# Optimization experiments

Hardware: AMD Instinct MI355X
Metric: run time of the kernel (lower is better)

Reference implementation:

```python
import jax, jax.numpy as jnp
import numpy as np

VIOL_TOL = 12.0
CLASH_TOL = 1.5
C_N_LEN = (1.329, 1.341)        # (non-proline, proline)
C_N_STD = (0.014, 0.016)
CA_C_N = (-0.5203, 0.0353)      # (gt cos, stddev)
C_N_CA = (-0.4473, 0.0311)
EPS = 1e-6


def setup_inputs() -> dict:
    key = jax.random.key(0)
    k = jax.random.split(key, 6)
    B, N = 1, 512
    pos = jax.random.normal(k[0], (B, N, 14, 3), jnp.float32) * 5.0
    atom_mask = jnp.ones((B, N, 14), jnp.float32)
    residue_types = jax.random.randint(k[1], (B, N), 0, 21, dtype=jnp.int32)
    residue_index = jnp.broadcast_to(jnp.arange(N, dtype=jnp.int32)[None], (B, N))
    vdw_table = jax.random.uniform(k[2], (21, 14), jnp.float32, 1.0, 2.0)
    lower_bound_table = jax.random.uniform(k[3], (21, 14, 14), jnp.float32, 1.0, 2.0)
    upper_bound_table = lower_bound_table + jax.random.uniform(k[4], (21, 14, 14), jnp.float32, 0.5, 1.5)
    return {
        'predicted_positions': pos,
        'atom_mask': atom_mask,
        'residue_types': residue_types,
        'residue_index': residue_index,
        'vdw_table': vdw_table,
        'lower_bound_table': lower_bound_table,
        'upper_bound_table': upper_bound_table,
    }


def _bond_angle_losses(pos, atom_mask, residue_types, residue_index):
    f32 = pos.dtype
    this_ca, this_ca_m = pos[:, :-1, 1, :], atom_mask[:, :-1, 1]
    this_c, this_c_m = pos[:, :-1, 2, :], atom_mask[:, :-1, 2]
    next_n, next_n_m = pos[:, 1:, 0, :], atom_mask[:, 1:, 0]
    next_ca, next_ca_m = pos[:, 1:, 1, :], atom_mask[:, 1:, 1]
    no_gap = (residue_index[:, 1:] - residue_index[:, :-1] == 1).astype(f32)

    c_n_len = jnp.sqrt(jnp.sum((this_c - next_n) ** 2, -1) + EPS)
    pro = (residue_types[:, 1:] == 14).astype(f32)
    gt_len = (1.0 - pro) * C_N_LEN[0] + pro * C_N_LEN[1]
    gt_std = (1.0 - pro) * C_N_STD[0] + pro * C_N_STD[1]
    c_n_mask = this_c_m * next_n_m * no_gap
    c_n_err = jnp.sqrt((c_n_len - gt_len) ** 2 + EPS)
    c_n_loss = jnp.sum(c_n_mask * jax.nn.relu(c_n_err - VIOL_TOL * gt_std), -1) / (jnp.sum(c_n_mask, -1) + EPS)

    ca_c_len = jnp.sqrt(jnp.sum((this_ca - this_c) ** 2, -1) + EPS)
    n_ca_len = jnp.sqrt(jnp.sum((next_n - next_ca) ** 2, -1) + EPS)
    c_ca_u = (this_ca - this_c) / ca_c_len[..., None]
    c_n_u = (next_n - this_c) / c_n_len[..., None]
    n_ca_u = (next_ca - next_n) / n_ca_len[..., None]

    ca_c_n = jnp.sum(c_ca_u * c_n_u, -1)
    ca_c_n_mask = this_ca_m * this_c_m * next_n_m * no_gap
    ca_c_n_err = jnp.sqrt((ca_c_n - CA_C_N[0]) ** 2 + EPS)
    ca_c_n_loss = jnp.sum(ca_c_n_mask * jax.nn.relu(ca_c_n_err - VIOL_TOL * CA_C_N[1]), -1) / (jnp.sum(ca_c_n_mask, -1) + EPS)

    c_n_ca = jnp.sum(-c_n_u * n_ca_u, -1)
    c_n_ca_mask = this_c_m * next_n_m * next_ca_m * no_gap
    c_n_ca_err = jnp.sqrt((c_n_ca - C_N_CA[0]) ** 2 + EPS)
    c_n_ca_loss = jnp.sum(c_n_ca_mask * jax.nn.relu(c_n_ca_err - VIOL_TOL * C_N_CA[1]), -1) / (jnp.sum(c_n_ca_mask, -1) + EPS)

    return c_n_loss, ca_c_n_loss, c_n_ca_loss


def _clash_per_atom(pos, atom_mask, residue_types, residue_index, vdw_table):
    f32 = pos.dtype
    B, N = pos.shape[:2]
    A = N * 14
    pos_f = pos.reshape(B, A, 3)
    m_f = atom_mask.reshape(B, A)
    rt = jnp.minimum(residue_types, 20)
    vdw_f = vdw_table[rt].reshape(B, A)  # gather [B,N,14] -> flat

    diff = pos_f[:, :, None, :] - pos_f[:, None, :, :]
    dist = jnp.sqrt(jnp.sum(diff ** 2, -1) + 1e-8)  # [B,A,A]

    pair = m_f[:, :, None] * m_f[:, None, :]
    ari = jnp.repeat(residue_index, 14, axis=1)  # atom residue index [B,A]
    pair = pair * (ari[:, :, None] < ari[:, None, :]).astype(f32)

    slot = jnp.tile(jnp.arange(14), N)[None]  # [1,A]
    rtf = jnp.repeat(residue_types, 14, axis=1)
    c_n_bond = ((slot[:, :, None] == 2) & (slot[:, None, :] == 0) & (ari[:, None, :] - ari[:, :, None] == 1)) | \
               ((slot[:, :, None] == 0) & (slot[:, None, :] == 2) & (ari[:, :, None] - ari[:, None, :] == 1))
    disulfide = (rtf[:, :, None] == 4) & (rtf[:, None, :] == 4) & (slot[:, :, None] == 5) & (slot[:, None, :] == 5)
    pair = pair * (~c_n_bond).astype(f32) * (~disulfide).astype(f32)

    vdw_sum = vdw_f[:, :, None] + vdw_f[:, None, :]
    clash = jax.nn.relu(vdw_sum - CLASH_TOL - dist) * pair
    per_atom = (jnp.sum(clash, axis=1) + jnp.sum(clash, axis=2)).reshape(B, N, 14)
    return per_atom


def _within_per_atom(pos, atom_mask, residue_types, lower_bound_table, upper_bound_table):
    f32 = pos.dtype
    rt = jnp.minimum(residue_types, 20)
    lb = lower_bound_table[rt]  # [B,N,14,14]
    ub = upper_bound_table[rt]
    d = jnp.sqrt(jnp.sum((pos[:, :, :, None, :] - pos[:, :, None, :, :]) ** 2, -1) + 1e-8)
    pair = atom_mask[:, :, :, None] * atom_mask[:, :, None, :]
    pair = pair * (1.0 - jnp.eye(14, dtype=f32)[None, None])
    pair = pair * ((lb > 0.0) | (ub > 0.0)).astype(f32)
    loss = (jax.nn.relu(lb - d) + jax.nn.relu(d - ub)) * pair
    return jnp.sum(loss, axis=-2) + jnp.sum(loss, axis=-1)  # [B,N,14]


def reference(predicted_positions, atom_mask, residue_types, residue_index,
              vdw_table, lower_bound_table, upper_bound_table):
    c_n, ca_c_n, c_n_ca = _bond_angle_losses(predicted_positions, atom_mask, residue_types, residue_index)
    clash_pa = _clash_per_atom(predicted_positions, atom_mask, residue_types, residue_index, vdw_table)
    within_pa = _within_per_atom(predicted_positions, atom_mask, residue_types, lower_bound_table, upper_bound_table)
    num_atoms = jnp.clip(jnp.sum(atom_mask, axis=(1, 2)), 1e-6, None)
    clash_loss = jnp.sum(clash_pa + within_pa, axis=(1, 2)) / num_atoms
    return c_n + ca_c_n + c_n_ca + clash_loss
```

## Files before the change

kernel.cpp:

```cpp
#include <hip/hip_runtime.h>

#define EPS 1e-6f
#define IT 512
#define JTL 64
#define RATIO 8
#define WB 64

static __device__ __forceinline__ float wave_reduce_add(float v) {
#pragma unroll
    for (int o = 32; o > 0; o >>= 1) v += __shfl_down(v, o, 64);
    return v;
}


__device__ void do_bonds(const float* __restrict__ P, const float* __restrict__ M,
                         const int* __restrict__ RT, const int* __restrict__ RI,
                         float* __restrict__ Wtail, int N) {
    float n0 = 0.f, de0 = 0.f, n1 = 0.f, de1 = 0.f, n2 = 0.f, de2 = 0.f;
    for (int i = threadIdx.x; i < N - 1; i += blockDim.x) {
        float no_gap = (RI[i + 1] - RI[i] == 1) ? 1.f : 0.f;
        const float* ca0 = P + i * 42 + 3;
        const float* c0  = P + i * 42 + 6;
        const float* nn  = P + (i + 1) * 42 + 0;
        const float* ca1 = P + (i + 1) * 42 + 3;
        float m_ca0 = M[i * 14 + 1], m_c0 = M[i * 14 + 2];
        float m_nn = M[(i + 1) * 14 + 0], m_ca1 = M[(i + 1) * 14 + 1];

        float bx = nn[0] - c0[0], by = nn[1] - c0[1], bz = nn[2] - c0[2];
        float c_n_len = sqrtf(bx * bx + by * by + bz * bz + EPS);
        float pro = (RT[i + 1] == 14) ? 1.f : 0.f;
        float gt_len = (1.f - pro) * 1.329f + pro * 1.341f;
        float gt_std = (1.f - pro) * 0.014f + pro * 0.016f;
        float cnm = m_c0 * m_nn * no_gap;
        float dl = c_n_len - gt_len;
        float cne = sqrtf(dl * dl + EPS);
        n0 += cnm * fmaxf(cne - 12.f * gt_std, 0.f);
        de0 += cnm;

        float ax = ca0[0] - c0[0], ay = ca0[1] - c0[1], az = ca0[2] - c0[2];
        float ca_c_len = sqrtf(ax * ax + ay * ay + az * az + EPS);
        float ex = ca1[0] - nn[0], ey = ca1[1] - nn[1], ez = ca1[2] - nn[2];
        float n_ca_len = sqrtf(ex * ex + ey * ey + ez * ez + EPS);
        float inv_cn = 1.f / c_n_len, inv_ac = 1.f / ca_c_len, inv_nc = 1.f / n_ca_len;
        float ux = bx * inv_cn, uy = by * inv_cn, uz = bz * inv_cn;
        float cx = ax * inv_ac, cy = ay * inv_ac, cz = az * inv_ac;
        float wx = ex * inv_nc, wy = ey * inv_nc, wz = ez * inv_nc;

        float cacn = cx * ux + cy * uy + cz * uz;
        float m1 = m_ca0 * m_c0 * m_nn * no_gap;
        float t1 = cacn + 0.5203f;
        float e1 = sqrtf(t1 * t1 + EPS);
        n1 += m1 * fmaxf(e1 - 12.f * 0.0353f, 0.f);
        de1 += m1;

        float cnca = -(ux * wx + uy * wy + uz * wz);
        float m2 = m_c0 * m_nn * m_ca1 * no_gap;
        float t2 = cnca + 0.4473f;
        float e2 = sqrtf(t2 * t2 + EPS);
        n2 += m2 * fmaxf(e2 - 12.f * 0.0311f, 0.f);
        de2 += m2;
    }
    n0 = wave_reduce_add(n0); de0 = wave_reduce_add(de0);
    n1 = wave_reduce_add(n1); de1 = wave_reduce_add(de1);
    n2 = wave_reduce_add(n2); de2 = wave_reduce_add(de2);
    __shared__ float red[24];
    int lane = threadIdx.x & 63, wid = threadIdx.x >> 6;
    if (lane == 0) {
        red[wid * 6 + 0] = n0; red[wid * 6 + 1] = de0; red[wid * 6 + 2] = n1;
        red[wid * 6 + 3] = de1; red[wid * 6 + 4] = n2; red[wid * 6 + 5] = de2;
    }
    __syncthreads();
    if (threadIdx.x < 6) {
        Wtail[threadIdx.x] = red[threadIdx.x] + red[6 + threadIdx.x]
                           + red[12 + threadIdx.x] + red[18 + threadIdx.x];
    }
}

__device__ void do_within(const float* __restrict__ pos, const float* __restrict__ am,
                          const int* __restrict__ rtypes,
                          const float* __restrict__ lbt, const float* __restrict__ ubt,
                          float* __restrict__ slot, int N, int b, int wblk) {
    int total = N * 196;
    float sum = 0.f;
    for (int idx = wblk * blockDim.x + threadIdx.x; idx < total; idx += WB * blockDim.x) {
        int n = idx / 196;
        int p = idx - n * 196;
        int i = p / 14;
        int j = p - i * 14;
        if (i == j) continue;
        size_t bn = (size_t)b * N + n;
        int rt = rtypes[bn]; rt = rt < 20 ? rt : 20;
        const float* pi = pos + bn * 42 + i * 3;
        const float* pj = pos + bn * 42 + j * 3;
        float dx = pi[0] - pj[0], dy = pi[1] - pj[1], dz = pi[2] - pj[2];
        float d = sqrtf(dx * dx + dy * dy + dz * dz + 1e-8f);
        float lb = lbt[rt * 196 + p], ub = ubt[rt * 196 + p];
        float gate = (lb > 0.f || ub > 0.f) ? 1.f : 0.f;
        float m = am[bn * 14 + i] * am[bn * 14 + j] * gate;
        sum += (fmaxf(lb - d, 0.f) + fmaxf(d - ub, 0.f)) * m;
    }
    sum = wave_reduce_add(sum);
    __shared__ float red2[4];
    int lane = threadIdx.x & 63, wid = threadIdx.x >> 6;
    if (lane == 0) red2[wid] = sum;
    __syncthreads();
    if (threadIdx.x == 0) *slot = red2[0] + red2[1] + red2[2] + red2[3];
}

__device__ void do_clash(const float* __restrict__ P, const float* __restrict__ M,
                         const int* __restrict__ RT, const int* __restrict__ RI,
                         const float* __restrict__ vdw, float* __restrict__ slot,
                         int N, int A, int TJ, int p) {
    int bi = 0, rem = p;
    while (true) {
        int cnt = TJ - RATIO * bi;
        cnt = cnt > 0 ? cnt : 0;
        if (rem < cnt) break;
        rem -= cnt; ++bi;
    }
    int bj = RATIO * bi + rem;

    __shared__ float4 sPos[JTL];
    __shared__ float sMask[JTL];
    __shared__ int sRI[JTL];
    __shared__ int sMeta[JTL];

    int t = threadIdx.x;
    if (t < JTL) {
        int j = bj * JTL + t;
        if (j < A) {
            int res = j / 14;
            int sl = j - res * 14;
            int rt = RT[res];
            int rtc = rt < 20 ? rt : 20;
            sPos[t] = make_float4(P[j * 3], P[j * 3 + 1], P[j * 3 + 2],
                                  vdw[rtc * 14 + sl] - 1.5f);
            sMask[t] = M[j];
            sRI[t] = RI[res];
            sMeta[t] = sl | (((rt == 4) && (sl == 5)) ? 16 : 0);
        } else {
            sPos[t] = make_float4(1e30f, 1e30f, 1e30f, -1e30f);
            sMask[t] = 0.f; sRI[t] = 0x7fffffff; sMeta[t] = 0;
        }
    }
    __syncthreads();

    int i0 = bi * IT + t;
    int i1 = i0 + 256;
    float xi0 = 0.f, yi0 = 0.f, zi0 = 0.f, vi0 = -1e30f, mi0 = 0.f;
    float xi1 = 0.f, yi1 = 0.f, zi1 = 0.f, vi1 = -1e30f, mi1 = 0.f;
    int iri0 = 0, iri1 = 0;
    bool icys0 = false, icys1 = false;
    int isl0 = -1, isl1 = -1;
    if (i0 < A) {
        int res = i0 / 14; isl0 = i0 - res * 14;
        int rt = RT[res]; int rtc = rt < 20 ? rt : 20;
        vi0 = vdw[rtc * 14 + isl0];
        xi0 = P[i0 * 3]; yi0 = P[i0 * 3 + 1]; zi0 = P[i0 * 3 + 2];
        mi0 = M[i0]; iri0 = RI[res]; icys0 = (rt == 4) && (isl0 == 5);
        if (mi0 == 0.f) vi0 = -1e30f;
    }
    if (i1 < A) {
        int res = i1 / 14; isl1 = i1 - res * 14;
        int rt = RT[res]; int rtc = rt < 20 ? rt : 20;
        vi1 = vdw[rtc * 14 + isl1];
        xi1 = P[i1 * 3]; yi1 = P[i1 * 3 + 1]; zi1 = P[i1 * 3 + 2];
        mi1 = M[i1]; iri1 = RI[res]; icys1 = (rt == 4) && (isl1 == 5);
        if (mi1 == 0.f) vi1 = -1e30f;
    }

    float sum = 0.f;
    int jbase_g = bj * JTL;
    for (int base = 0; base < JTL; base += 8) {
        float4 r[8];
#pragma unroll
        for (int k = 0; k < 8; ++k) r[k] = sPos[base + k];
#pragma unroll
        for (int k = 0; k < 8; ++k) {
            float w = r[k].w;
            {
                float dx = xi0 - r[k].x, dy = yi0 - r[k].y, dz = zi0 - r[k].z;
                float d2 = dx * dx + dy * dy + dz * dz;
                float s = vi0 + w;
                if (s > 0.f && d2 < s * s) {
                    int jj = base + k, jg = jbase_g + jj;
                    if (i0 < jg) {
                        int jri = sRI[jj];
                        if (iri0 != jri) {
                            int dj = jri - iri0;
                            int jm = sMeta[jj], jsl = jm & 15;
                            bool cn = (isl0 == 2 && jsl == 0 && dj == 1) ||
                                      (isl0 == 0 && jsl == 2 && dj == -1);
                            bool ssb = icys0 && (jm & 16);
                            if (!cn && !ssb)
                                sum += (s - sqrtf(d2 + 1e-8f)) * mi0 * sMask[jj];
                        }
                    }
                }
            }
            {
                float dx = xi1 - r[k].x, dy = yi1 - r[k].y, dz = zi1 - r[k].z;
                float d2 = dx * dx + dy * dy + dz * dz;
                float s = vi1 + w;
                if (s > 0.f && d2 < s * s) {
                    int jj = base + k, jg = jbase_g + jj;
                    if (i1 < jg) {
                        int jri = sRI[jj];
                        if (iri1 != jri) {
                            int dj = jri - iri1;
                            int jm = sMeta[jj], jsl = jm & 15;
                            bool cn = (isl1 == 2 && jsl == 0 && dj == 1) ||
                                      (isl1 == 0 && jsl == 2 && dj == -1);
                            bool ssb = icys1 && (jm & 16);
                            if (!cn && !ssb)
                                sum += (s - sqrtf(d2 + 1e-8f)) * mi1 * sMask[jj];
                        }
                    }
                }
            }
        }
    }
    sum = wave_reduce_add(sum);
    __shared__ float red3[4];
    int lane = t & 63, wid = t >> 6;
    if (lane == 0) red3[wid] = sum;
    __syncthreads();
    if (t == 0) *slot = red3[0] + red3[1] + red3[2] + red3[3];
}

__global__ __launch_bounds__(256, 4) void main_kernel(
        const float* __restrict__ pos, const float* __restrict__ am,
        const int* __restrict__ rtypes, const int* __restrict__ rindex,
        const float* __restrict__ vdw, const float* __restrict__ lbt,
        const float* __restrict__ ubt, float* __restrict__ ws,
        int N, int A, int TJ, int CB, int NBP, int stride) {
    int b = blockIdx.y;
    const float* P = pos + (size_t)b * A * 3;
    const float* M = am + (size_t)b * A;
    const int* RT = rtypes + (size_t)b * N;
    const int* RI = rindex + (size_t)b * N;
    float* W = ws + (size_t)b * stride;
    int bid = blockIdx.x;
    if (bid < CB) {
        do_clash(P, M, RT, RI, vdw, &W[bid], N, A, TJ, bid);
    } else if (bid < NBP) {
        do_within(pos, am, rtypes, lbt, ubt, &W[bid], N, b, bid - CB);
    } else {
        do_bonds(P, M, RT, RI, &W[NBP], N);
    }
}

__global__ __launch_bounds__(256) void final_kernel(
        const float* __restrict__ am, const float* __restrict__ ws,
        float* __restrict__ out, int N, int NBP, int stride) {
    int b = blockIdx.x;
    const float* M = am + (size_t)b * N * 14;
    const float* W = ws + (size_t)b * stride;
    float s = 0.f, pairs = 0.f;
    int A = N * 14;
    int A4 = A >> 2;
    const float4* M4 = (const float4*)M;
    for (int i = threadIdx.x; i < A4; i += blockDim.x) {
        float4 v = M4[i];
        s += v.x + v.y + v.z + v.w;
    }
    for (int i = A4 << 2; i < A; ++i) if (threadIdx.x == 0) s += M[i];
    for (int i = threadIdx.x; i < NBP; i += blockDim.x) pairs += W[i];
    s = wave_reduce_add(s);
    pairs = wave_reduce_add(pairs);
    __shared__ float red[8];
    int lane = threadIdx.x & 63, wid = threadIdx.x >> 6;
    if (lane == 0) { red[wid] = s; red[4 + wid] = pairs; }
    __syncthreads();
    if (threadIdx.x == 0) {
        float na = fmaxf(red[0] + red[1] + red[2] + red[3], 1e-6f);
        float P2 = red[4] + red[5] + red[6] + red[7];
        const float* T6 = W + NBP;
        float loss = T6[0] / (T6[1] + EPS) + T6[2] / (T6[3] + EPS)
                   + T6[4] / (T6[5] + EPS) + 2.f * P2 / na;
        out[b] = loss;
    }
}

extern "C" void kernel_launch(void* const* d_in, const int* in_sizes, int n_in,
                              void* d_out, int out_size, void* d_ws, size_t ws_size,
                              hipStream_t stream) {
    const float* pos = (const float*)d_in[0];
    const float* am = (const float*)d_in[1];
    const int* rtypes = (const int*)d_in[2];
    const int* rindex = (const int*)d_in[3];
    const float* vdw = (const float*)d_in[4];
    const float* lbt = (const float*)d_in[5];
    const float* ubt = (const float*)d_in[6];
    float* out = (float*)d_out;
    float* ws = (float*)d_ws;

    int B = out_size;
    int N = in_sizes[2] / B;
    int A = N * 14;
    int TI = (A + IT - 1) / IT;
    int TJ = (A + JTL - 1) / JTL;
    int CB = 0;
    for (int bi = 0; bi < TI; ++bi) {
        int c = TJ - RATIO * bi;
        if (c > 0) CB += c;
    }
    int NBP = CB + WB;
    int stride = NBP + 6;

    dim3 grid(NBP + 1, B);
    main_kernel<<<grid, 256, 0, stream>>>(pos, am, rtypes, rindex, vdw, lbt, ubt,
                                          ws, N, A, TJ, CB, NBP, stride);
    final_kernel<<<B, 256, 0, stream>>>(am, ws, out, N, NBP, stride);
}
```

Measured before the change: 89.59 us.

## Fuse final reduction into main kernel via cooperative grid sync

Replaces the two-kernel launch with one cooperative kernel. All blocks sync on the grid, then block 0 does the final reduction, which removes the second launch and its gap. The atom-mask sum moves into the bonds block, and the clash tile packs residue index and metadata into one shared int. Masked j atoms now get a -1e30 radius so they are culled early. The cost is a grid-wide barrier and a cooperative launch, which requires every block to be resident at once.

```diff
diff --git a/kernel.cpp b/kernel.cpp
--- a/kernel.cpp
+++ b/kernel.cpp
@@ -1,4 +1,7 @@
 #include <hip/hip_runtime.h>
+#include <hip/hip_cooperative_groups.h>
+
+namespace cg = cooperative_groups;
 
 #define EPS 1e-6f
 #define IT 512
@@ -15,7 +18,7 @@
 
 __device__ void do_bonds(const float* __restrict__ P, const float* __restrict__ M,
                          const int* __restrict__ RT, const int* __restrict__ RI,
-                         float* __restrict__ Wtail, int N) {
+                         float* __restrict__ Wtail, int N, int A) {
     float n0 = 0.f, de0 = 0.f, n1 = 0.f, de1 = 0.f, n2 = 0.f, de2 = 0.f;
     for (int i = threadIdx.x; i < N - 1; i += blockDim.x) {
         float no_gap = (RI[i + 1] - RI[i] == 1) ? 1.f : 0.f;
@@ -60,19 +63,30 @@
         n2 += m2 * fmaxf(e2 - 12.f * 0.0311f, 0.f);
         de2 += m2;
     }
+    float ms = 0.f;
+    int A4 = A >> 2;
+    const float4* M4 = (const float4*)M;
+    for (int i = threadIdx.x; i < A4; i += blockDim.x) {
+        float4 v = M4[i];
+        ms += v.x + v.y + v.z + v.w;
+    }
+    if (threadIdx.x == 0) for (int i = A4 << 2; i < A; ++i) ms += M[i];
+
     n0 = wave_reduce_add(n0); de0 = wave_reduce_add(de0);
     n1 = wave_reduce_add(n1); de1 = wave_reduce_add(de1);
     n2 = wave_reduce_add(n2); de2 = wave_reduce_add(de2);
-    __shared__ float red[24];
+    ms = wave_reduce_add(ms);
+    __shared__ float redb[28];
     int lane = threadIdx.x & 63, wid = threadIdx.x >> 6;
     if (lane == 0) {
-        red[wid * 6 + 0] = n0; red[wid * 6 + 1] = de0; red[wid * 6 + 2] = n1;
-        red[wid * 6 + 3] = de1; red[wid * 6 + 4] = n2; red[wid * 6 + 5] = de2;
+        redb[wid * 7 + 0] = n0; redb[wid * 7 + 1] = de0; redb[wid * 7 + 2] = n1;
+        redb[wid * 7 + 3] = de1; redb[wid * 7 + 4] = n2; redb[wid * 7 + 5] = de2;
+        redb[wid * 7 + 6] = ms;
     }
     __syncthreads();
-    if (threadIdx.x < 6) {
-        Wtail[threadIdx.x] = red[threadIdx.x] + red[6 + threadIdx.x]
-                           + red[12 + threadIdx.x] + red[18 + threadIdx.x];
+    if (threadIdx.x < 7) {
+        Wtail[threadIdx.x] = redb[threadIdx.x] + redb[7 + threadIdx.x]
+                           + redb[14 + threadIdx.x] + redb[21 + threadIdx.x];
     }
 }
 
@@ -122,8 +136,7 @@
 
     __shared__ float4 sPos[JTL];
     __shared__ float sMask[JTL];
-    __shared__ int sRI[JTL];
-    __shared__ int sMeta[JTL];
+    __shared__ int sRM[JTL];
 
     int t = threadIdx.x;
     if (t < JTL) {
@@ -133,14 +146,14 @@
             int sl = j - res * 14;
             int rt = RT[res];
             int rtc = rt < 20 ? rt : 20;
-            sPos[t] = make_float4(P[j * 3], P[j * 3 + 1], P[j * 3 + 2],
-                                  vdw[rtc * 14 + sl] - 1.5f);
-            sMask[t] = M[j];
-            sRI[t] = RI[res];
-            sMeta[t] = sl | (((rt == 4) && (sl == 5)) ? 16 : 0);
+            float mj = M[j];
+            float w = (mj == 0.f) ? -1e30f : (vdw[rtc * 14 + sl] - 1.5f);
+            sPos[t] = make_float4(P[j * 3], P[j * 3 + 1], P[j * 3 + 2], w);
+            sMask[t] = mj;
+            sRM[t] = (RI[res] << 5) | sl | (((rt == 4) && (sl == 5)) ? 16 : 0);
         } else {
             sPos[t] = make_float4(1e30f, 1e30f, 1e30f, -1e30f);
-            sMask[t] = 0.f; sRI[t] = 0x7fffffff; sMeta[t] = 0;
+            sMask[t] = 0.f; sRM[t] = 0;
         }
     }
     __syncthreads();
@@ -185,13 +198,14 @@
                 if (s > 0.f && d2 < s * s) {
                     int jj = base + k, jg = jbase_g + jj;
                     if (i0 < jg) {
-                        int jri = sRI[jj];
+                        int rm = sRM[jj];
+                        int jri = rm >> 5;
                         if (iri0 != jri) {
                             int dj = jri - iri0;
-                            int jm = sMeta[jj], jsl = jm & 15;
+                            int jsl = rm & 15;
                             bool cn = (isl0 == 2 && jsl == 0 && dj == 1) ||
                                       (isl0 == 0 && jsl == 2 && dj == -1);
-                            bool ssb = icys0 && (jm & 16);
+                            bool ssb = icys0 && (rm & 16);
                             if (!cn && !ssb)
                                 sum += (s - sqrtf(d2 + 1e-8f)) * mi0 * sMask[jj];
                         }
@@ -205,13 +219,14 @@
                 if (s > 0.f && d2 < s * s) {
                     int jj = base + k, jg = jbase_g + jj;
                     if (i1 < jg) {
-                        int jri = sRI[jj];
+                        int rm = sRM[jj];
+                        int jri = rm >> 5;
                         if (iri1 != jri) {
                             int dj = jri - iri1;
-                            int jm = sMeta[jj], jsl = jm & 15;
+                            int jsl = rm & 15;
                             bool cn = (isl1 == 2 && jsl == 0 && dj == 1) ||
                                       (isl1 == 0 && jsl == 2 && dj == -1);
-                            bool ssb = icys1 && (jm & 16);
+                            bool ssb = icys1 && (rm & 16);
                             if (!cn && !ssb)
                                 sum += (s - sqrtf(d2 + 1e-8f)) * mi1 * sMask[jj];
                         }
@@ -228,11 +243,12 @@
     if (t == 0) *slot = red3[0] + red3[1] + red3[2] + red3[3];
 }
 
-__global__ __launch_bounds__(256, 4) void main_kernel(
+__global__ __launch_bounds__(256, 4) void fused_kernel(
         const float* __restrict__ pos, const float* __restrict__ am,
         const int* __restrict__ rtypes, const int* __restrict__ rindex,
         const float* __restrict__ vdw, const float* __restrict__ lbt,
         const float* __restrict__ ubt, float* __restrict__ ws,
+        float* __restrict__ out,
         int N, int A, int TJ, int CB, int NBP, int stride) {
     int b = blockIdx.y;
     const float* P = pos + (size_t)b * A * 3;
@@ -246,39 +262,28 @@
     } else if (bid < NBP) {
         do_within(pos, am, rtypes, lbt, ubt, &W[bid], N, b, bid - CB);
     } else {
-        do_bonds(P, M, RT, RI, &W[NBP], N);
-    }
-}
-
-__global__ __launch_bounds__(256) void final_kernel(
-        const float* __restrict__ am, const float* __restrict__ ws,
-        float* __restrict__ out, int N, int NBP, int stride) {
-    int b = blockIdx.x;
-    const float* M = am + (size_t)b * N * 14;
-    const float* W = ws + (size_t)b * stride;
-    float s = 0.f, pairs = 0.f;
-    int A = N * 14;
-    int A4 = A >> 2;
-    const float4* M4 = (const float4*)M;
-    for (int i = threadIdx.x; i < A4; i += blockDim.x) {
-        float4 v = M4[i];
-        s += v.x + v.y + v.z + v.w;
-    }
-    for (int i = A4 << 2; i < A; ++i) if (threadIdx.x == 0) s += M[i];
-    for (int i = threadIdx.x; i < NBP; i += blockDim.x) pairs += W[i];
-    s = wave_reduce_add(s);
-    pairs = wave_reduce_add(pairs);
-    __shared__ float red[8];
-    int lane = threadIdx.x & 63, wid = threadIdx.x >> 6;
-    if (lane == 0) { red[wid] = s; red[4 + wid] = pairs; }
-    __syncthreads();
-    if (threadIdx.x == 0) {
-        float na = fmaxf(red[0] + red[1] + red[2] + red[3], 1e-6f);
-        float P2 = red[4] + red[5] + red[6] + red[7];
-        const float* T6 = W + NBP;
-        float loss = T6[0] / (T6[1] + EPS) + T6[2] / (T6[3] + EPS)
-                   + T6[4] / (T6[5] + EPS) + 2.f * P2 / na;
-        out[b] = loss;
+        do_bonds(P, M, RT, RI, &W[NBP], N, A);
+    }
+
+    __threadfence();
+    cg::this_grid().sync();
+
+    if (bid == 0) {
+        float pairs = 0.f;
+        for (int i = threadIdx.x; i < NBP; i += blockDim.x) pairs += W[i];
+        pairs = wave_reduce_add(pairs);
+        __shared__ float redf[4];
+        int lane = threadIdx.x & 63, wid = threadIdx.x >> 6;
+        if (lane == 0) redf[wid] = pairs;
+        __syncthreads();
+        if (threadIdx.x == 0) {
+            float P2 = redf[0] + redf[1] + redf[2] + redf[3];
+            const float* T7 = W + NBP;
+            float na = fmaxf(T7[6], 1e-6f);
+            float loss = T7[0] / (T7[1] + EPS) + T7[2] / (T7[3] + EPS)
+                       + T7[4] / (T7[5] + EPS) + 2.f * P2 / na;
+            out[b] = loss;
+        }
     }
 }
 
@@ -306,10 +311,13 @@
         if (c > 0) CB += c;
     }
     int NBP = CB + WB;
-    int stride = NBP + 6;
+    int stride = NBP + 7;
 
     dim3 grid(NBP + 1, B);
-    main_kernel<<<grid, 256, 0, stream>>>(pos, am, rtypes, rindex, vdw, lbt, ubt,
-                                          ws, N, A, TJ, CB, NBP, stride);
-    final_kernel<<<B, 256, 0, stream>>>(am, ws, out, N, NBP, stride);
-}
+    dim3 block(256);
+    void* args[] = {(void*)&pos, (void*)&am, (void*)&rtypes, (void*)&rindex,
+                    (void*)&vdw, (void*)&lbt, (void*)&ubt, (void*)&ws, (void*)&out,
+                    (void*)&N, (void*)&A, (void*)&TJ, (void*)&CB, (void*)&NBP,
+                    (void*)&stride};
+    hipLaunchCooperativeKernel((const void*)fused_kernel, grid, block, args, 0, stream);
+}
```

New measurement: 247.1 us. 176% more time.
